# Kernel tuning notes

Measured on AMD Instinct MI355X. Metric: run time of the kernel, lower is better.

Reference implementation:

```python
import jax, jax.numpy as jnp
import numpy as np

EPS_LEN = 1e-20
EPS_DENOM = 1e-6


def _dot(a, b):
    return jnp.sum(a * b, axis=-1, keepdims=True)


def _safe_normalize(x):
    return x / jnp.sqrt(jnp.maximum(_dot(x, x), EPS_LEN))


def _auto_normals(positions, faces):
    i0, i1, i2 = faces[:, 0], faces[:, 1], faces[:, 2]
    v0 = positions[i0]
    v1 = positions[i1]
    v2 = positions[i2]
    face_normals = jnp.cross(v1 - v0, v2 - v0)  # [F,3]
    v_nrm = jnp.zeros_like(positions)
    v_nrm = v_nrm.at[i0].add(face_normals)
    v_nrm = v_nrm.at[i1].add(face_normals)
    v_nrm = v_nrm.at[i2].add(face_normals)
    default = jnp.array([0.0, 0.0, 1.0], dtype=positions.dtype)
    v_nrm = jnp.where(_dot(v_nrm, v_nrm) > EPS_LEN, v_nrm, default)
    return _safe_normalize(v_nrm)


def _compute_tangents(positions, normals, faces, texcoords, uv_faces):
    pos = [positions[faces[:, i]] for i in range(3)]
    tex = [texcoords[uv_faces[:, i]] for i in range(3)]
    uve1 = tex[1] - tex[0]
    uve2 = tex[2] - tex[0]
    pe1 = pos[1] - pos[0]
    pe2 = pos[2] - pos[0]
    nom = pe1 * uve2[..., 1:2] - pe2 * uve1[..., 1:2]  # [F,3]
    denom = uve1[..., 0:1] * uve2[..., 1:2] - uve1[..., 1:2] * uve2[..., 0:1]
    denom = jnp.where(denom > 0.0,
                      jnp.maximum(denom, EPS_DENOM),
                      jnp.minimum(denom, -EPS_DENOM))
    tang = nom / denom  # [F,3]
    tangents = jnp.zeros_like(normals)
    for i in range(3):
        tangents = tangents.at[faces[:, i]].add(tang)
    tangents = _safe_normalize(tangents)
    tangents = _safe_normalize(tangents - _dot(tangents, normals) * normals)
    return tangents


def setup_inputs() -> dict:
    key = jax.random.key(0)
    k1, k2, k3, k4 = jax.random.split(key, 4)
    V, T, F = 2_000_000, 2_200_000, 4_000_000
    positions = jax.random.normal(k1, (V, 3), dtype=jnp.float32)
    faces = jax.random.randint(k2, (F, 3), 0, V, dtype=jnp.int32)
    texcoords = jax.random.uniform(k3, (T, 2), dtype=jnp.float32)
    uv_faces = jax.random.randint(k4, (F, 3), 0, T, dtype=jnp.int32)
    return {"positions": positions, "faces": faces,
            "texcoords": texcoords, "uv_faces": uv_faces}


def reference(positions, faces, texcoords, uv_faces):
    normals = _auto_normals(positions, faces)
    tangents = _compute_tangents(positions, normals, faces, texcoords, uv_faces)
    return jnp.stack([normals, tangents])  # [2, V, 3]
```

## Files before the change

### kernel.cpp

```cpp
#include <hip/hip_runtime.h>

#define EPS_LEN   1e-20f
#define EPS_DENOM 1e-6f

#define CB_LOG   13
#define CB       (1 << CB_LOG)
#define BLKA     1024
#define MAXB     256
#define CAP1     50176
#define CAP2     57344
#define FST      6
#define QLOG     11
#define QSIZE    (1 << QLOG)
#define VPT      (CB / BLKA)

__global__ __launch_bounds__(BLKA)
void vg_face_bin_pay(const float* __restrict__ pos, const int* __restrict__ faces,
                     const float* __restrict__ tex, const int* __restrict__ uvf,
                     float* __restrict__ en, float* __restrict__ et,
                     unsigned short* __restrict__ ev,
                     int* __restrict__ cursors, int* __restrict__ validw,
                     float* __restrict__ nacc, float* __restrict__ tacc,
                     int F, int NBC)
{
    __shared__ int h[MAXB], sc[MAXB], loff[MAXB], lfill[MAXB], gbase[MAXB];
    __shared__ float spnx[BLKA], spny[BLKA], spnz[BLKA];
    __shared__ float sptx[BLKA], spty[BLKA], sptz[BLKA];
    __shared__ unsigned short sfl[3 * BLKA];
    __shared__ unsigned short svloc[3 * BLKA];
    __shared__ unsigned char  sbuck[3 * BLKA];

    const int t = threadIdx.x;
    const int f = blockIdx.x * BLKA + t;

    if (t < MAXB) { h[t] = 0; lfill[t] = 0; }
    for (int i = t; i < 3 * BLKA; i += BLKA) sbuck[i] = 0xFF;
    __syncthreads();

    const bool on = (f < F);
    int i0 = 0, i1 = 0, i2 = 0;
    float nx = 0, ny = 0, nz = 0, txv = 0, tyv = 0, tzv = 0;

    if (on) {
        i0 = faces[3 * f + 0]; i1 = faces[3 * f + 1]; i2 = faces[3 * f + 2];

        const float p0x = pos[3*i0+0], p0y = pos[3*i0+1], p0z = pos[3*i0+2];
        const float p1x = pos[3*i1+0], p1y = pos[3*i1+1], p1z = pos[3*i1+2];
        const float p2x = pos[3*i2+0], p2y = pos[3*i2+1], p2z = pos[3*i2+2];

        const float e1x = p1x - p0x, e1y = p1y - p0y, e1z = p1z - p0z;
        const float e2x = p2x - p0x, e2y = p2y - p0y, e2z = p2z - p0z;

        nx = e1y * e2z - e1z * e2y;
        ny = e1z * e2x - e1x * e2z;
        nz = e1x * e2y - e1y * e2x;

        const int t0 = uvf[3 * f + 0];
        const int t1 = uvf[3 * f + 1];
        const int t2 = uvf[3 * f + 2];

        const float u0x = tex[2*t0+0], u0y = tex[2*t0+1];
        const float u1x = tex[2*t1+0], u1y = tex[2*t1+1];
        const float u2x = tex[2*t2+0], u2y = tex[2*t2+1];

        const float d1x = u1x - u0x, d1y = u1y - u0y;
        const float d2x = u2x - u0x, d2y = u2y - u0y;

        float denom = d1x * d2y - d1y * d2x;
        denom = (denom > 0.0f) ? fmaxf(denom, EPS_DENOM) : fminf(denom, -EPS_DENOM);
        const float inv = 1.0f / denom;

        txv = (e1x * d2y - e2x * d1y) * inv;
        tyv = (e1y * d2y - e2y * d1y) * inv;
        tzv = (e1z * d2y - e2z * d1y) * inv;

        spnx[t] = nx;  spny[t] = ny;  spnz[t] = nz;
        sptx[t] = txv; spty[t] = tyv; sptz[t] = tzv;

        atomicAdd(&h[i0 >> CB_LOG], 1);
        atomicAdd(&h[i1 >> CB_LOG], 1);
        atomicAdd(&h[i2 >> CB_LOG], 1);
    }
    __syncthreads();

    if (t < MAXB) sc[t] = h[t];
    __syncthreads();
    for (int d = 1; d < MAXB; d <<= 1) {
        int v2 = 0;
        if (t < MAXB) v2 = sc[t] + ((t >= d) ? sc[t - d] : 0);
        __syncthreads();
        if (t < MAXB) sc[t] = v2;
        __syncthreads();
    }
    if (t < MAXB) {
        loff[t] = sc[t] - h[t];
        const int cnt = h[t];
        int gb = -1;
        if (t < NBC && cnt > 0) {
            gb = atomicAdd(&cursors[t], cnt);
            if (gb + cnt <= CAP1) atomicMax(&validw[t], gb + cnt);
            else gb = -1;
        }
        gbase[t] = gb;
    }
    __syncthreads();

    if (on) {
        const int vi[3] = { i0, i1, i2 };
#pragma unroll
        for (int c = 0; c < 3; ++c) {
            const int v = vi[c];
            const int b = v >> CB_LOG;
            if (gbase[b] >= 0) {
                const int slot = atomicAdd(&lfill[b], 1);
                const int p = loff[b] + slot;
                sfl[p]   = (unsigned short)t;
                svloc[p] = (unsigned short)(v & (CB - 1));
                sbuck[p] = (unsigned char)b;
            } else {
                atomicAdd(&nacc[3*v+0], nx);
                atomicAdd(&nacc[3*v+1], ny);
                atomicAdd(&nacc[3*v+2], nz);
                atomicAdd(&tacc[3*v+0], txv);
                atomicAdd(&tacc[3*v+1], tyv);
                atomicAdd(&tacc[3*v+2], tzv);
            }
        }
    }
    __syncthreads();

    for (int i = t; i < 3 * BLKA; i += BLKA) {
        const unsigned b = sbuck[i];
        if (b != 0xFFu) {
            const int g = gbase[b] + (i - loff[b]);
            const size_t s = (size_t)b * CAP1 + g;
            const int fl = sfl[i];
            float* pn = &en[s * 3];
            pn[0] = spnx[fl]; pn[1] = spny[fl]; pn[2] = spnz[fl];
            float* pt = &et[s * 3];
            pt[0] = sptx[fl]; pt[1] = spty[fl]; pt[2] = sptz[fl];
            ev[s] = svloc[i];
        }
    }
}

__global__ __launch_bounds__(BLKA)
void vg_reduce_pay(const float* __restrict__ en, const float* __restrict__ et,
                   const unsigned short* __restrict__ ev,
                   const int* __restrict__ validw,
                   float* __restrict__ nacc, float* __restrict__ tacc,
                   int V)
{
    __shared__ float acc[CB * 3];
    const int b = blockIdx.x;
    const int t = threadIdx.x;
    int count = validw[b];
    if (count > CAP1) count = CAP1;
    const size_t ebase = (size_t)b * CAP1;
    const int vbase = b << CB_LOG;

    float nreg[VPT][3];

    for (int i = t; i < CB * 3; i += BLKA) acc[i] = 0.0f;
    __syncthreads();

    for (int e = t; e < count; e += BLKA) {
        const int vloc = (int)ev[ebase + e];
        const float* p = &en[(ebase + e) * 3];
        float* a = &acc[vloc * 3];
        atomicAdd(a + 0, p[0]);
        atomicAdd(a + 1, p[1]);
        atomicAdd(a + 2, p[2]);
    }
    __syncthreads();

#pragma unroll
    for (int k = 0; k < VPT; ++k) {
        const int i = t + k * BLKA;
        const int v = vbase + i;
        float nx = 0.0f, ny = 0.0f, nz = 1.0f;
        if (v < V) {
            nx = nacc[3*v+0] + acc[3*i+0];
            ny = nacc[3*v+1] + acc[3*i+1];
            nz = nacc[3*v+2] + acc[3*i+2];
            const float nd = nx*nx + ny*ny + nz*nz;
            if (nd > EPS_LEN) {
                const float invn = 1.0f / sqrtf(nd);
                nx *= invn; ny *= invn; nz *= invn;
            } else {
                nx = 0.0f; ny = 0.0f; nz = 1.0f;
            }
            nacc[3*v+0] = nx; nacc[3*v+1] = ny; nacc[3*v+2] = nz;
        }
        nreg[k][0] = nx; nreg[k][1] = ny; nreg[k][2] = nz;
    }
    __syncthreads();

    for (int i = t; i < CB * 3; i += BLKA) acc[i] = 0.0f;
    __syncthreads();

    for (int e = t; e < count; e += BLKA) {
        const int vloc = (int)ev[ebase + e];
        const float* p = &et[(ebase + e) * 3];
        float* a = &acc[vloc * 3];
        atomicAdd(a + 0, p[0]);
        atomicAdd(a + 1, p[1]);
        atomicAdd(a + 2, p[2]);
    }
    __syncthreads();

#pragma unroll
    for (int k = 0; k < VPT; ++k) {
        const int i = t + k * BLKA;
        const int v = vbase + i;
        if (v < V) {
            float tx = tacc[3*v+0] + acc[3*i+0];
            float ty = tacc[3*v+1] + acc[3*i+1];
            float tz = tacc[3*v+2] + acc[3*i+2];
            const float nx = nreg[k][0], ny = nreg[k][1], nz = nreg[k][2];

            const float td = tx*tx + ty*ty + tz*tz;
            const float invt = 1.0f / sqrtf(fmaxf(td, EPS_LEN));
            tx *= invt; ty *= invt; tz *= invt;

            const float dp = tx*nx + ty*ny + tz*nz;
            tx -= dp * nx; ty -= dp * ny; tz -= dp * nz;

            const float td2 = tx*tx + ty*ty + tz*tz;
            const float invt2 = 1.0f / sqrtf(fmaxf(td2, EPS_LEN));
            tx *= invt2; ty *= invt2; tz *= invt2;

            tacc[3*v+0] = tx; tacc[3*v+1] = ty; tacc[3*v+2] = tz;
        }
    }
}

__global__ __launch_bounds__(BLKA)
void vg_face_bin3(const float* __restrict__ pos, const int* __restrict__ faces,
                  const float* __restrict__ tex, const int* __restrict__ uvf,
                  float* __restrict__ face_data,
                  unsigned* __restrict__ ef, unsigned short* __restrict__ ev,
                  int* __restrict__ cursors, int* __restrict__ validw,
                  float* __restrict__ nacc, float* __restrict__ tacc,
                  int F, int NBC)
{
    __shared__ int h[MAXB], sc[MAXB], loff[MAXB], lfill[MAXB], gbase[MAXB];
    __shared__ unsigned       sface[3 * BLKA];
    __shared__ unsigned short svloc[3 * BLKA];
    __shared__ unsigned char  sbuck[3 * BLKA];

    const int t = threadIdx.x;
    const int f = blockIdx.x * BLKA + t;

    if (t < MAXB) { h[t] = 0; lfill[t] = 0; }
    for (int i = t; i < 3 * BLKA; i += BLKA) sbuck[i] = 0xFF;
    __syncthreads();

    const bool on = (f < F);
    int i0 = 0, i1 = 0, i2 = 0;
    float nx = 0, ny = 0, nz = 0, txv = 0, tyv = 0, tzv = 0;

    if (on) {
        i0 = faces[3 * f + 0]; i1 = faces[3 * f + 1]; i2 = faces[3 * f + 2];

        const float p0x = pos[3*i0+0], p0y = pos[3*i0+1], p0z = pos[3*i0+2];
        const float p1x = pos[3*i1+0], p1y = pos[3*i1+1], p1z = pos[3*i1+2];
        const float p2x = pos[3*i2+0], p2y = pos[3*i2+1], p2z = pos[3*i2+2];

        const float e1x = p1x - p0x, e1y = p1y - p0y, e1z = p1z - p0z;
        const float e2x = p2x - p0x, e2y = p2y - p0y, e2z = p2z - p0z;

        nx = e1y * e2z - e1z * e2y;
        ny = e1z * e2x - e1x * e2z;
        nz = e1x * e2y - e1y * e2x;

        const int t0 = uvf[3 * f + 0];
        const int t1 = uvf[3 * f + 1];
        const int t2 = uvf[3 * f + 2];

        const float u0x = tex[2*t0+0], u0y = tex[2*t0+1];
        const float u1x = tex[2*t1+0], u1y = tex[2*t1+1];
        const float u2x = tex[2*t2+0], u2y = tex[2*t2+1];

        const float d1x = u1x - u0x, d1y = u1y - u0y;
        const float d2x = u2x - u0x, d2y = u2y - u0y;

        float denom = d1x * d2y - d1y * d2x;
        denom = (denom > 0.0f) ? fmaxf(denom, EPS_DENOM) : fminf(denom, -EPS_DENOM);
        const float inv = 1.0f / denom;

        txv = (e1x * d2y - e2x * d1y) * inv;
        tyv = (e1y * d2y - e2y * d1y) * inv;
        tzv = (e1z * d2y - e2z * d1y) * inv;

        float* fd = &face_data[(size_t)f * FST];
        reinterpret_cast<float2*>(fd)[0] = make_float2(nx, ny);
        reinterpret_cast<float2*>(fd)[1] = make_float2(nz, txv);
        reinterpret_cast<float2*>(fd)[2] = make_float2(tyv, tzv);

        atomicAdd(&h[i0 >> CB_LOG], 1);
        atomicAdd(&h[i1 >> CB_LOG], 1);
        atomicAdd(&h[i2 >> CB_LOG], 1);
    }
    __syncthreads();

    if (t < MAXB) sc[t] = h[t];
    __syncthreads();
    for (int d = 1; d < MAXB; d <<= 1) {
        int v2 = 0;
        if (t < MAXB) v2 = sc[t] + ((t >= d) ? sc[t - d] : 0);
        __syncthreads();
        if (t < MAXB) sc[t] = v2;
        __syncthreads();
    }
    if (t < MAXB) {
        loff[t] = sc[t] - h[t];
        const int cnt = h[t];
        int gb = -1;
        if (t < NBC && cnt > 0) {
            gb = atomicAdd(&cursors[t], cnt);
            if (gb + cnt <= CAP2) atomicMax(&validw[t], gb + cnt);
            else gb = -1;
        }
        gbase[t] = gb;
    }
    __syncthreads();

    if (on) {
        const int vi[3] = { i0, i1, i2 };
#pragma unroll
        for (int c = 0; c < 3; ++c) {
            const int v = vi[c];
            const int b = v >> CB_LOG;
            if (gbase[b] >= 0) {
                const int slot = atomicAdd(&lfill[b], 1);
                const int p = loff[b] + slot;
                sface[p] = (unsigned)f;
                svloc[p] = (unsigned short)(v & (CB - 1));
                sbuck[p] = (unsigned char)b;
            } else {
                atomicAdd(&nacc[3*v+0], nx);
                atomicAdd(&nacc[3*v+1], ny);
                atomicAdd(&nacc[3*v+2], nz);
                atomicAdd(&tacc[3*v+0], txv);
                atomicAdd(&tacc[3*v+1], tyv);
                atomicAdd(&tacc[3*v+2], tzv);
            }
        }
    }
    __syncthreads();

    for (int i = t; i < 3 * BLKA; i += BLKA) {
        const unsigned b = sbuck[i];
        if (b != 0xFFu) {
            const int g = gbase[b] + (i - loff[b]);
            const size_t base = (size_t)b * CAP2;
            ef[base + g] = sface[i];
            ev[base + g] = svloc[i];
        }
    }
}

__global__ __launch_bounds__(BLKA)
void vg_bucket_reduce3(const float* __restrict__ face_data,
                       const unsigned* __restrict__ ef,
                       const unsigned short* __restrict__ ev,
                       const int* __restrict__ validw,
                       float* __restrict__ nacc, float* __restrict__ tacc,
                       int V)
{
    __shared__ float acc[QSIZE * 6];
    const int b = blockIdx.x;
    const int t = threadIdx.x;
    int count = validw[b];
    if (count > CAP2) count = CAP2;
    const size_t ebase = (size_t)b * CAP2;
    const int vbase = b << CB_LOG;

    for (int q = 0; q < 4; ++q) {
        for (int i = t; i < QSIZE * 6; i += BLKA) acc[i] = 0.0f;
        __syncthreads();

        for (int e = t; e < count; e += BLKA) {
            const int vloc = (int)ev[ebase + e];
            if ((vloc >> QLOG) == q) {
                const unsigned f = ef[ebase + e];
                const float* fd = &face_data[(size_t)f * FST];
                const float2 a0 = reinterpret_cast<const float2*>(fd)[0];
                const float2 a1 = reinterpret_cast<const float2*>(fd)[1];
                const float2 a2 = reinterpret_cast<const float2*>(fd)[2];
                float* a = &acc[(vloc & (QSIZE - 1)) * 6];
                atomicAdd(a + 0, a0.x);
                atomicAdd(a + 1, a0.y);
                atomicAdd(a + 2, a1.x);
                atomicAdd(a + 3, a1.y);
                atomicAdd(a + 4, a2.x);
                atomicAdd(a + 5, a2.y);
            }
        }
        __syncthreads();

        for (int i = t; i < QSIZE; i += BLKA) {
            const int v = vbase + (q << QLOG) + i;
            if (v < V) {
                float nx = nacc[3*v+0] + acc[i*6+0];
                float ny = nacc[3*v+1] + acc[i*6+1];
                float nz = nacc[3*v+2] + acc[i*6+2];
                float tx = tacc[3*v+0] + acc[i*6+3];
                float ty = tacc[3*v+1] + acc[i*6+4];
                float tz = tacc[3*v+2] + acc[i*6+5];

                const float nd = nx*nx + ny*ny + nz*nz;
                if (nd > EPS_LEN) {
                    const float invn = 1.0f / sqrtf(nd);
                    nx *= invn; ny *= invn; nz *= invn;
                } else {
                    nx = 0.0f; ny = 0.0f; nz = 1.0f;
                }

                const float td = tx*tx + ty*ty + tz*tz;
                const float invt = 1.0f / sqrtf(fmaxf(td, EPS_LEN));
                tx *= invt; ty *= invt; tz *= invt;

                const float dp = tx*nx + ty*ny + tz*nz;
                tx -= dp * nx; ty -= dp * ny; tz -= dp * nz;

                const float td2 = tx*tx + ty*ty + tz*tz;
                const float invt2 = 1.0f / sqrtf(fmaxf(td2, EPS_LEN));
                tx *= invt2; ty *= invt2; tz *= invt2;

                nacc[3*v+0] = nx; nacc[3*v+1] = ny; nacc[3*v+2] = nz;
                tacc[3*v+0] = tx; tacc[3*v+1] = ty; tacc[3*v+2] = tz;
            }
        }
        __syncthreads();
    }
}

__global__ void vg_face_kernel(const float* __restrict__ pos,
                               const int*   __restrict__ faces,
                               const float* __restrict__ tex,
                               const int*   __restrict__ uvf,
                               float* __restrict__ nacc,
                               float* __restrict__ tacc,
                               int F) {
    int f = blockIdx.x * blockDim.x + threadIdx.x;
    if (f >= F) return;

    const int i0 = faces[3*f+0], i1 = faces[3*f+1], i2 = faces[3*f+2];

    const float p0x = pos[3*i0+0], p0y = pos[3*i0+1], p0z = pos[3*i0+2];
    const float p1x = pos[3*i1+0], p1y = pos[3*i1+1], p1z = pos[3*i1+2];
    const float p2x = pos[3*i2+0], p2y = pos[3*i2+1], p2z = pos[3*i2+2];

    const float e1x = p1x - p0x, e1y = p1y - p0y, e1z = p1z - p0z;
    const float e2x = p2x - p0x, e2y = p2y - p0y, e2z = p2z - p0z;

    const float nx = e1y*e2z - e1z*e2y;
    const float ny = e1z*e2x - e1x*e2z;
    const float nz = e1x*e2y - e1y*e2x;

    const int t0 = uvf[3*f+0], t1 = uvf[3*f+1], t2 = uvf[3*f+2];

    const float u0x = tex[2*t0+0], u0y = tex[2*t0+1];
    const float u1x = tex[2*t1+0], u1y = tex[2*t1+1];
    const float u2x = tex[2*t2+0], u2y = tex[2*t2+1];

    const float d1x = u1x - u0x, d1y = u1y - u0y;
    const float d2x = u2x - u0x, d2y = u2y - u0y;

    float denom = d1x * d2y - d1y * d2x;
    denom = (denom > 0.0f) ? fmaxf(denom, EPS_DENOM) : fminf(denom, -EPS_DENOM);
    const float inv = 1.0f / denom;

    const float tx = (e1x*d2y - e2x*d1y) * inv;
    const float ty = (e1y*d2y - e2y*d1y) * inv;
    const float tz = (e1z*d2y - e2z*d1y) * inv;

    atomicAdd(&nacc[3*i0+0], nx); atomicAdd(&nacc[3*i0+1], ny); atomicAdd(&nacc[3*i0+2], nz);
    atomicAdd(&nacc[3*i1+0], nx); atomicAdd(&nacc[3*i1+1], ny); atomicAdd(&nacc[3*i1+2], nz);
    atomicAdd(&nacc[3*i2+0], nx); atomicAdd(&nacc[3*i2+1], ny); atomicAdd(&nacc[3*i2+2], nz);
    atomicAdd(&tacc[3*i0+0], tx); atomicAdd(&tacc[3*i0+1], ty); atomicAdd(&tacc[3*i0+2], tz);
    atomicAdd(&tacc[3*i1+0], tx); atomicAdd(&tacc[3*i1+1], ty); atomicAdd(&tacc[3*i1+2], tz);
    atomicAdd(&tacc[3*i2+0], tx); atomicAdd(&tacc[3*i2+1], ty); atomicAdd(&tacc[3*i2+2], tz);
}

__global__ void vg_finalize_kernel(float* __restrict__ nacc,
                                   float* __restrict__ tacc,
                                   int V) {
    int v = blockIdx.x * blockDim.x + threadIdx.x;
    if (v >= V) return;

    float nx = nacc[3*v+0], ny = nacc[3*v+1], nz = nacc[3*v+2];
    float nd = nx*nx + ny*ny + nz*nz;
    if (nd > EPS_LEN) {
        const float invn = 1.0f / sqrtf(nd);
        nx *= invn; ny *= invn; nz *= invn;
    } else {
        nx = 0.0f; ny = 0.0f; nz = 1.0f;
    }

    float tx = tacc[3*v+0], ty = tacc[3*v+1], tz = tacc[3*v+2];
    float td = tx*tx + ty*ty + tz*tz;
    float invt = 1.0f / sqrtf(fmaxf(td, EPS_LEN));
    tx *= invt; ty *= invt; tz *= invt;
    const float dp = tx*nx + ty*ny + tz*nz;
    tx -= dp*nx; ty -= dp*ny; tz -= dp*nz;
    float td2 = tx*tx + ty*ty + tz*tz;
    float invt2 = 1.0f / sqrtf(fmaxf(td2, EPS_LEN));
    tx *= invt2; ty *= invt2; tz *= invt2;

    nacc[3*v+0] = nx; nacc[3*v+1] = ny; nacc[3*v+2] = nz;
    tacc[3*v+0] = tx; tacc[3*v+1] = ty; tacc[3*v+2] = tz;
}

extern "C" void kernel_launch(void* const* d_in, const int* in_sizes, int n_in,
                              void* d_out, int out_size, void* d_ws, size_t ws_size,
                              hipStream_t stream) {
    const float* pos   = (const float*)d_in[0];
    const int*   faces = (const int*)  d_in[1];
    const float* tex   = (const float*)d_in[2];
    const int*   uvf   = (const int*)  d_in[3];

    const int V = in_sizes[0] / 3;
    const int F = in_sizes[1] / 3;

    float* out  = (float*)d_out;
    float* nacc = out;
    float* tacc = out + (size_t)3 * V;

    const int NBC = (V + CB - 1) >> CB_LOG;
    const size_t cur_b = (size_t)NBC * sizeof(int);

    hipMemsetAsync(d_out, 0, (size_t)out_size * sizeof(float), stream);

    const size_t NE1   = (size_t)NBC * CAP1;
    const size_t en_b  = (NE1 * 12 + 255) & ~(size_t)255;
    const size_t et_b  = (NE1 * 12 + 255) & ~(size_t)255;
    const size_t ev1_b = (NE1 * 2 + 255) & ~(size_t)255;
    const size_t need1 = en_b + et_b + ev1_b + 2 * cur_b + 256;

    if (ws_size >= need1 && NBC <= 255) {
        char* ws = (char*)d_ws;
        float*          en  = (float*)ws;                ws += en_b;
        float*          et  = (float*)ws;                ws += et_b;
        unsigned short* ev  = (unsigned short*)ws;       ws += ev1_b;
        int*            cursors = (int*)ws;
        int*            validw  = cursors + NBC;

        hipMemsetAsync(cursors, 0, 2 * cur_b, stream);

        vg_face_bin_pay<<<(F + BLKA - 1) / BLKA, BLKA, 0, stream>>>(
            pos, faces, tex, uvf, en, et, ev, cursors, validw, nacc, tacc, F, NBC);
        vg_reduce_pay<<<NBC, BLKA, 0, stream>>>(
            en, et, ev, validw, nacc, tacc, V);
        return;
    }

    const size_t NE2    = (size_t)NBC * CAP2;
    const size_t face_b = ((size_t)F * FST * sizeof(float) + 255) & ~(size_t)255;
    const size_t ef_b   = (NE2 * 4 + 255) & ~(size_t)255;
    const size_t ev2_b  = (NE2 * 2 + 255) & ~(size_t)255;
    const size_t need2  = face_b + ef_b + ev2_b + 2 * cur_b + 256;

    if (ws_size >= need2 && NBC <= 255 && F < (1 << 22)) {
        char* ws = (char*)d_ws;
        float*          face_data = (float*)ws;          ws += face_b;
        unsigned*       ef        = (unsigned*)ws;       ws += ef_b;
        unsigned short* ev        = (unsigned short*)ws; ws += ev2_b;
        int*            cursors   = (int*)ws;
        int*            validw    = cursors + NBC;

        hipMemsetAsync(cursors, 0, 2 * cur_b, stream);

        vg_face_bin3<<<(F + BLKA - 1) / BLKA, BLKA, 0, stream>>>(
            pos, faces, tex, uvf, face_data, ef, ev, cursors, validw,
            nacc, tacc, F, NBC);
        vg_bucket_reduce3<<<NBC, BLKA, 0, stream>>>(
            face_data, ef, ev, validw, nacc, tacc, V);
        return;
    }

    const int BLK = 256;
    vg_face_kernel<<<(F + BLK - 1) / BLK, BLK, 0, stream>>>(pos, faces, tex, uvf,
                                                            nacc, tacc, F);
    vg_finalize_kernel<<<(V + BLK - 1) / BLK, BLK, 0, stream>>>(nacc, tacc, V);
}
```

Baseline: 936.1 us.

## Use finer vertex buckets with chunked face passes and a fused normal/tangent reduce

```diff
diff --git a/kernel.cpp b/kernel.cpp
--- a/kernel.cpp
+++ b/kernel.cpp
@@ -3,41 +3,45 @@
 #define EPS_LEN   1e-20f
 #define EPS_DENOM 1e-6f
 
-#define CB_LOG   13
+#define CB_LOG   11
 #define CB       (1 << CB_LOG)
 #define BLKA     1024
-#define MAXB     256
-#define CAP1     50176
+#define MAXB     1024
+#define NCHUNK   2
+#define CAPC     6528
+
+#define CB2_LOG  13
+#define CB2      (1 << CB2_LOG)
+#define MAXB2    256
 #define CAP2     57344
 #define FST      6
 #define QLOG     11
 #define QSIZE    (1 << QLOG)
-#define VPT      (CB / BLKA)
 
 __global__ __launch_bounds__(BLKA)
-void vg_face_bin_pay(const float* __restrict__ pos, const int* __restrict__ faces,
-                     const float* __restrict__ tex, const int* __restrict__ uvf,
-                     float* __restrict__ en, float* __restrict__ et,
-                     unsigned short* __restrict__ ev,
-                     int* __restrict__ cursors, int* __restrict__ validw,
-                     float* __restrict__ nacc, float* __restrict__ tacc,
-                     int F, int NBC)
+void vg_face_bin_c(const float* __restrict__ pos, const int* __restrict__ faces,
+                   const float* __restrict__ tex, const int* __restrict__ uvf,
+                   float* __restrict__ en, float* __restrict__ et,
+                   unsigned short* __restrict__ ev,
+                   int* __restrict__ cursors, int* __restrict__ validw,
+                   float* __restrict__ nacc, float* __restrict__ tacc,
+                   int f0, int f1, int NBC)
 {
     __shared__ int h[MAXB], sc[MAXB], loff[MAXB], lfill[MAXB], gbase[MAXB];
     __shared__ float spnx[BLKA], spny[BLKA], spnz[BLKA];
     __shared__ float sptx[BLKA], spty[BLKA], sptz[BLKA];
     __shared__ unsigned short sfl[3 * BLKA];
     __shared__ unsigned short svloc[3 * BLKA];
-    __shared__ unsigned char  sbuck[3 * BLKA];
+    __shared__ unsigned short sbuck[3 * BLKA];
 
     const int t = threadIdx.x;
-    const int f = blockIdx.x * BLKA + t;
-
-    if (t < MAXB) { h[t] = 0; lfill[t] = 0; }
-    for (int i = t; i < 3 * BLKA; i += BLKA) sbuck[i] = 0xFF;
-    __syncthreads();
-
-    const bool on = (f < F);
+    const int f = f0 + blockIdx.x * BLKA + t;
+
+    h[t] = 0; lfill[t] = 0;
+    for (int i = t; i < 3 * BLKA; i += BLKA) sbuck[i] = 0xFFFFu;
+    __syncthreads();
+
+    const bool on = (f < f1);
     int i0 = 0, i1 = 0, i2 = 0;
     float nx = 0, ny = 0, nz = 0, txv = 0, tyv = 0, tzv = 0;
 
@@ -83,22 +87,21 @@
     }
     __syncthreads();
 
-    if (t < MAXB) sc[t] = h[t];
+    sc[t] = h[t];
     __syncthreads();
     for (int d = 1; d < MAXB; d <<= 1) {
-        int v2 = 0;
-        if (t < MAXB) v2 = sc[t] + ((t >= d) ? sc[t - d] : 0);
-        __syncthreads();
-        if (t < MAXB) sc[t] = v2;
-        __syncthreads();
-    }
-    if (t < MAXB) {
+        const int v2 = sc[t] + ((t >= d) ? sc[t - d] : 0);
+        __syncthreads();
+        sc[t] = v2;
+        __syncthreads();
+    }
+    {
         loff[t] = sc[t] - h[t];
         const int cnt = h[t];
         int gb = -1;
         if (t < NBC && cnt > 0) {
             gb = atomicAdd(&cursors[t], cnt);
-            if (gb + cnt <= CAP1) atomicMax(&validw[t], gb + cnt);
+            if (gb + cnt <= CAPC) atomicMax(&validw[t], gb + cnt);
             else gb = -1;
         }
         gbase[t] = gb;
@@ -116,7 +119,7 @@
                 const int p = loff[b] + slot;
                 sfl[p]   = (unsigned short)t;
                 svloc[p] = (unsigned short)(v & (CB - 1));
-                sbuck[p] = (unsigned char)b;
+                sbuck[p] = (unsigned short)b;
             } else {
                 atomicAdd(&nacc[3*v+0], nx);
                 atomicAdd(&nacc[3*v+1], ny);
@@ -131,105 +134,86 @@
 
     for (int i = t; i < 3 * BLKA; i += BLKA) {
         const unsigned b = sbuck[i];
-        if (b != 0xFFu) {
+        if (b != 0xFFFFu) {
             const int g = gbase[b] + (i - loff[b]);
-            const size_t s = (size_t)b * CAP1 + g;
+            const size_t s = (size_t)b * CAPC + g;
             const int fl = sfl[i];
-            float* pn = &en[s * 3];
-            pn[0] = spnx[fl]; pn[1] = spny[fl]; pn[2] = spnz[fl];
-            float* pt = &et[s * 3];
-            pt[0] = sptx[fl]; pt[1] = spty[fl]; pt[2] = sptz[fl];
+            en[s*3+0] = spnx[fl]; en[s*3+1] = spny[fl]; en[s*3+2] = spnz[fl];
+            et[s*3+0] = sptx[fl]; et[s*3+1] = spty[fl]; et[s*3+2] = sptz[fl];
             ev[s] = svloc[i];
         }
     }
 }
 
 __global__ __launch_bounds__(BLKA)
-void vg_reduce_pay(const float* __restrict__ en, const float* __restrict__ et,
-                   const unsigned short* __restrict__ ev,
-                   const int* __restrict__ validw,
-                   float* __restrict__ nacc, float* __restrict__ tacc,
-                   int V)
+void vg_reduce_c(const float* __restrict__ en, const float* __restrict__ et,
+                 const unsigned short* __restrict__ ev,
+                 const int* __restrict__ validw,
+                 float* __restrict__ nacc, float* __restrict__ tacc,
+                 int V, int isFinal)
 {
-    __shared__ float acc[CB * 3];
+    __shared__ float accn[CB * 3];
+    __shared__ float acct[CB * 3];
     const int b = blockIdx.x;
     const int t = threadIdx.x;
+
+    for (int i = t; i < CB * 3; i += BLKA) { accn[i] = 0.0f; acct[i] = 0.0f; }
+    __syncthreads();
+
     int count = validw[b];
-    if (count > CAP1) count = CAP1;
-    const size_t ebase = (size_t)b * CAP1;
-    const int vbase = b << CB_LOG;
-
-    float nreg[VPT][3];
-
-    for (int i = t; i < CB * 3; i += BLKA) acc[i] = 0.0f;
-    __syncthreads();
+    if (count > CAPC) count = CAPC;
+    const size_t ebase = (size_t)b * CAPC;
 
     for (int e = t; e < count; e += BLKA) {
         const int vloc = (int)ev[ebase + e];
-        const float* p = &en[(ebase + e) * 3];
-        float* a = &acc[vloc * 3];
-        atomicAdd(a + 0, p[0]);
-        atomicAdd(a + 1, p[1]);
-        atomicAdd(a + 2, p[2]);
-    }
-    __syncthreads();
-
+        const float* pn = &en[(ebase + e) * 3];
+        const float* pt = &et[(ebase + e) * 3];
+        float* an = &accn[vloc * 3];
+        float* at = &acct[vloc * 3];
+        atomicAdd(an + 0, pn[0]);
+        atomicAdd(an + 1, pn[1]);
+        atomicAdd(an + 2, pn[2]);
+        atomicAdd(at + 0, pt[0]);
+        atomicAdd(at + 1, pt[1]);
+        atomicAdd(at + 2, pt[2]);
+    }
+    __syncthreads();
+
+    const int vbase = b << CB_LOG;
 #pragma unroll
-    for (int k = 0; k < VPT; ++k) {
-        const int i = t + k * BLKA;
-        const int v = vbase + i;
-        float nx = 0.0f, ny = 0.0f, nz = 1.0f;
-        if (v < V) {
-            nx = nacc[3*v+0] + acc[3*i+0];
-            ny = nacc[3*v+1] + acc[3*i+1];
-            nz = nacc[3*v+2] + acc[3*i+2];
-            const float nd = nx*nx + ny*ny + nz*nz;
-            if (nd > EPS_LEN) {
-                const float invn = 1.0f / sqrtf(nd);
-                nx *= invn; ny *= invn; nz *= invn;
-            } else {
-                nx = 0.0f; ny = 0.0f; nz = 1.0f;
-            }
-            nacc[3*v+0] = nx; nacc[3*v+1] = ny; nacc[3*v+2] = nz;
-        }
-        nreg[k][0] = nx; nreg[k][1] = ny; nreg[k][2] = nz;
-    }
-    __syncthreads();
-
-    for (int i = t; i < CB * 3; i += BLKA) acc[i] = 0.0f;
-    __syncthreads();
-
-    for (int e = t; e < count; e += BLKA) {
-        const int vloc = (int)ev[ebase + e];
-        const float* p = &et[(ebase + e) * 3];
-        float* a = &acc[vloc * 3];
-        atomicAdd(a + 0, p[0]);
-        atomicAdd(a + 1, p[1]);
-        atomicAdd(a + 2, p[2]);
-    }
-    __syncthreads();
-
-#pragma unroll
-    for (int k = 0; k < VPT; ++k) {
-        const int i = t + k * BLKA;
+    for (int k = 0; k < CB; k += BLKA) {
+        const int i = t + k;
         const int v = vbase + i;
         if (v < V) {
-            float tx = tacc[3*v+0] + acc[3*i+0];
-            float ty = tacc[3*v+1] + acc[3*i+1];
-            float tz = tacc[3*v+2] + acc[3*i+2];
-            const float nx = nreg[k][0], ny = nreg[k][1], nz = nreg[k][2];
-
-            const float td = tx*tx + ty*ty + tz*tz;
-            const float invt = 1.0f / sqrtf(fmaxf(td, EPS_LEN));
-            tx *= invt; ty *= invt; tz *= invt;
-
-            const float dp = tx*nx + ty*ny + tz*nz;
-            tx -= dp * nx; ty -= dp * ny; tz -= dp * nz;
-
-            const float td2 = tx*tx + ty*ty + tz*tz;
-            const float invt2 = 1.0f / sqrtf(fmaxf(td2, EPS_LEN));
-            tx *= invt2; ty *= invt2; tz *= invt2;
-
+            float nx = nacc[3*v+0] + accn[3*i+0];
+            float ny = nacc[3*v+1] + accn[3*i+1];
+            float nz = nacc[3*v+2] + accn[3*i+2];
+            float tx = tacc[3*v+0] + acct[3*i+0];
+            float ty = tacc[3*v+1] + acct[3*i+1];
+            float tz = tacc[3*v+2] + acct[3*i+2];
+
+            if (isFinal) {
+                const float nd = nx*nx + ny*ny + nz*nz;
+                if (nd > EPS_LEN) {
+                    const float invn = 1.0f / sqrtf(nd);
+                    nx *= invn; ny *= invn; nz *= invn;
+                } else {
+                    nx = 0.0f; ny = 0.0f; nz = 1.0f;
+                }
+
+                const float td = tx*tx + ty*ty + tz*tz;
+                const float invt = 1.0f / sqrtf(fmaxf(td, EPS_LEN));
+                tx *= invt; ty *= invt; tz *= invt;
+
+                const float dp = tx*nx + ty*ny + tz*nz;
+                tx -= dp * nx; ty -= dp * ny; tz -= dp * nz;
+
+                const float td2 = tx*tx + ty*ty + tz*tz;
+                const float invt2 = 1.0f / sqrtf(fmaxf(td2, EPS_LEN));
+                tx *= invt2; ty *= invt2; tz *= invt2;
+            }
+
+            nacc[3*v+0] = nx; nacc[3*v+1] = ny; nacc[3*v+2] = nz;
             tacc[3*v+0] = tx; tacc[3*v+1] = ty; tacc[3*v+2] = tz;
         }
     }
@@ -244,7 +228,7 @@
                   float* __restrict__ nacc, float* __restrict__ tacc,
                   int F, int NBC)
 {
-    __shared__ int h[MAXB], sc[MAXB], loff[MAXB], lfill[MAXB], gbase[MAXB];
+    __shared__ int h[MAXB2], sc[MAXB2], loff[MAXB2], lfill[MAXB2], gbase[MAXB2];
     __shared__ unsigned       sface[3 * BLKA];
     __shared__ unsigned short svloc[3 * BLKA];
     __shared__ unsigned char  sbuck[3 * BLKA];
@@ -252,7 +236,7 @@
     const int t = threadIdx.x;
     const int f = blockIdx.x * BLKA + t;
 
-    if (t < MAXB) { h[t] = 0; lfill[t] = 0; }
+    if (t < MAXB2) { h[t] = 0; lfill[t] = 0; }
     for (int i = t; i < 3 * BLKA; i += BLKA) sbuck[i] = 0xFF;
     __syncthreads();
 
@@ -298,22 +282,22 @@
         reinterpret_cast<float2*>(fd)[1] = make_float2(nz, txv);
         reinterpret_cast<float2*>(fd)[2] = make_float2(tyv, tzv);
 
-        atomicAdd(&h[i0 >> CB_LOG], 1);
-        atomicAdd(&h[i1 >> CB_LOG], 1);
-        atomicAdd(&h[i2 >> CB_LOG], 1);
-    }
-    __syncthreads();
-
-    if (t < MAXB) sc[t] = h[t];
-    __syncthreads();
-    for (int d = 1; d < MAXB; d <<= 1) {
+        atomicAdd(&h[i0 >> CB2_LOG], 1);
+        atomicAdd(&h[i1 >> CB2_LOG], 1);
+        atomicAdd(&h[i2 >> CB2_LOG], 1);
+    }
+    __syncthreads();
+
+    if (t < MAXB2) sc[t] = h[t];
+    __syncthreads();
+    for (int d = 1; d < MAXB2; d <<= 1) {
         int v2 = 0;
-        if (t < MAXB) v2 = sc[t] + ((t >= d) ? sc[t - d] : 0);
-        __syncthreads();
-        if (t < MAXB) sc[t] = v2;
-        __syncthreads();
-    }
-    if (t < MAXB) {
+        if (t < MAXB2) v2 = sc[t] + ((t >= d) ? sc[t - d] : 0);
+        __syncthreads();
+        if (t < MAXB2) sc[t] = v2;
+        __syncthreads();
+    }
+    if (t < MAXB2) {
         loff[t] = sc[t] - h[t];
         const int cnt = h[t];
         int gb = -1;
@@ -331,12 +315,12 @@
 #pragma unroll
         for (int c = 0; c < 3; ++c) {
             const int v = vi[c];
-            const int b = v >> CB_LOG;
+            const int b = v >> CB2_LOG;
             if (gbase[b] >= 0) {
                 const int slot = atomicAdd(&lfill[b], 1);
                 const int p = loff[b] + slot;
                 sface[p] = (unsigned)f;
-                svloc[p] = (unsigned short)(v & (CB - 1));
+                svloc[p] = (unsigned short)(v & (CB2 - 1));
                 sbuck[p] = (unsigned char)b;
             } else {
                 atomicAdd(&nacc[3*v+0], nx);
@@ -375,7 +359,7 @@
     int count = validw[b];
     if (count > CAP2) count = CAP2;
     const size_t ebase = (size_t)b * CAP2;
-    const int vbase = b << CB_LOG;
+    const int vbase = b << CB2_LOG;
 
     for (int q = 0; q < 4; ++q) {
         for (int i = t; i < QSIZE * 6; i += BLKA) acc[i] = 0.0f;
@@ -529,56 +513,74 @@
     float* nacc = out;
     float* tacc = out + (size_t)3 * V;
 
-    const int NBC = (V + CB - 1) >> CB_LOG;
-    const size_t cur_b = (size_t)NBC * sizeof(int);
-
     hipMemsetAsync(d_out, 0, (size_t)out_size * sizeof(float), stream);
 
-    const size_t NE1   = (size_t)NBC * CAP1;
-    const size_t en_b  = (NE1 * 12 + 255) & ~(size_t)255;
-    const size_t et_b  = (NE1 * 12 + 255) & ~(size_t)255;
-    const size_t ev1_b = (NE1 * 2 + 255) & ~(size_t)255;
-    const size_t need1 = en_b + et_b + ev1_b + 2 * cur_b + 256;
-
-    if (ws_size >= need1 && NBC <= 255) {
-        char* ws = (char*)d_ws;
-        float*          en  = (float*)ws;                ws += en_b;
-        float*          et  = (float*)ws;                ws += et_b;
-        unsigned short* ev  = (unsigned short*)ws;       ws += ev1_b;
-        int*            cursors = (int*)ws;
-        int*            validw  = cursors + NBC;
-
-        hipMemsetAsync(cursors, 0, 2 * cur_b, stream);
-
-        vg_face_bin_pay<<<(F + BLKA - 1) / BLKA, BLKA, 0, stream>>>(
-            pos, faces, tex, uvf, en, et, ev, cursors, validw, nacc, tacc, F, NBC);
-        vg_reduce_pay<<<NBC, BLKA, 0, stream>>>(
-            en, et, ev, validw, nacc, tacc, V);
-        return;
-    }
-
-    const size_t NE2    = (size_t)NBC * CAP2;
-    const size_t face_b = ((size_t)F * FST * sizeof(float) + 255) & ~(size_t)255;
-    const size_t ef_b   = (NE2 * 4 + 255) & ~(size_t)255;
-    const size_t ev2_b  = (NE2 * 2 + 255) & ~(size_t)255;
-    const size_t need2  = face_b + ef_b + ev2_b + 2 * cur_b + 256;
-
-    if (ws_size >= need2 && NBC <= 255 && F < (1 << 22)) {
-        char* ws = (char*)d_ws;
-        float*          face_data = (float*)ws;          ws += face_b;
-        unsigned*       ef        = (unsigned*)ws;       ws += ef_b;
-        unsigned short* ev        = (unsigned short*)ws; ws += ev2_b;
-        int*            cursors   = (int*)ws;
-        int*            validw    = cursors + NBC;
-
-        hipMemsetAsync(cursors, 0, 2 * cur_b, stream);
-
-        vg_face_bin3<<<(F + BLKA - 1) / BLKA, BLKA, 0, stream>>>(
-            pos, faces, tex, uvf, face_data, ef, ev, cursors, validw,
-            nacc, tacc, F, NBC);
-        vg_bucket_reduce3<<<NBC, BLKA, 0, stream>>>(
-            face_data, ef, ev, validw, nacc, tacc, V);
-        return;
+    const int NBC1 = (V + CB - 1) >> CB_LOG;
+    {
+        const size_t NE1   = (size_t)NBC1 * CAPC;
+        const size_t en_b  = (NE1 * 12 + 255) & ~(size_t)255;
+        const size_t et_b  = (NE1 * 12 + 255) & ~(size_t)255;
+        const size_t ev_b  = (NE1 * 2 + 255) & ~(size_t)255;
+        const size_t cur_b = ((size_t)NBC1 * sizeof(int) + 255) & ~(size_t)255;
+        const size_t need1 = en_b + et_b + ev_b + 2 * cur_b + 256;
+
+        if (ws_size >= need1 && NBC1 <= MAXB) {
+            char* ws = (char*)d_ws;
+            float*          en  = (float*)ws;          ws += en_b;
+            float*          et  = (float*)ws;          ws += et_b;
+            unsigned short* ev  = (unsigned short*)ws; ws += ev_b;
+            int*            cursors = (int*)ws;        ws += cur_b;
+            int*            validw  = (int*)ws;
+
+            const int Fc = (F + NCHUNK - 1) / NCHUNK;
+            for (int c = 0; c < NCHUNK; ++c) {
+                const int f0 = c * Fc;
+                const int f1 = (f0 + Fc < F) ? (f0 + Fc) : F;
+                if (f0 >= f1) continue;
+
+                hipMemsetAsync(cursors, 0, cur_b, stream);
+                hipMemsetAsync(validw,  0, cur_b, stream);
+
+                const int nblk = (f1 - f0 + BLKA - 1) / BLKA;
+                vg_face_bin_c<<<nblk, BLKA, 0, stream>>>(
+                    pos, faces, tex, uvf, en, et, ev, cursors, validw,
+                    nacc, tacc, f0, f1, NBC1);
+
+                const int isFinal = (f1 == F) ? 1 : 0;
+                vg_reduce_c<<<NBC1, BLKA, 0, stream>>>(
+                    en, et, ev, validw, nacc, tacc, V, isFinal);
+            }
+            return;
+        }
+    }
+
+    const int NBC2 = (V + CB2 - 1) >> CB2_LOG;
+    {
+        const size_t NE2    = (size_t)NBC2 * CAP2;
+        const size_t face_b = ((size_t)F * FST * sizeof(float) + 255) & ~(size_t)255;
+        const size_t ef_b   = (NE2 * 4 + 255) & ~(size_t)255;
+        const size_t ev2_b  = (NE2 * 2 + 255) & ~(size_t)255;
+        const size_t cur_b  = ((size_t)NBC2 * sizeof(int) + 255) & ~(size_t)255;
+        const size_t need2  = face_b + ef_b + ev2_b + 2 * cur_b + 256;
+
+        if (ws_size >= need2 && NBC2 <= 255 && F < (1 << 22)) {
+            char* ws = (char*)d_ws;
+            float*          face_data = (float*)ws;          ws += face_b;
+            unsigned*       ef        = (unsigned*)ws;       ws += ef_b;
+            unsigned short* ev        = (unsigned short*)ws; ws += ev2_b;
+            int*            cursors   = (int*)ws;            ws += cur_b;
+            int*            validw    = (int*)ws;
+
+            hipMemsetAsync(cursors, 0, cur_b, stream);
+            hipMemsetAsync(validw,  0, cur_b, stream);
+
+            vg_face_bin3<<<(F + BLKA - 1) / BLKA, BLKA, 0, stream>>>(
+                pos, faces, tex, uvf, face_data, ef, ev, cursors, validw,
+                nacc, tacc, F, NBC2);
+            vg_bucket_reduce3<<<NBC2, BLKA, 0, stream>>>(
+                face_data, ef, ev, validw, nacc, tacc, V);
+            return;
+        }
     }
 
     const int BLK = 256;
```

New measurement: 1.067 ms. 1.14x slower.
